# Kernel optimization log

Measured on AMD Instinct MI355X. Metric: run time of the kernel, lower is better.

## Reference

```python
import jax, jax.numpy as jnp
import numpy as np

EPS = 1e-5
STW = 10   # short_term_window_size
L = 12     # mlp_layers


def gru_step(h, x, Wi, Wh, bi, bh):
    # torch nn.GRU cell, gate order (r, z, n)
    gi = x @ Wi.T + bi            # [B, 3H]
    gh = h @ Wh.T + bh            # [B, 3H]
    ir, iz, inn = jnp.split(gi, 3, axis=-1)
    hr, hz, hn = jnp.split(gh, 3, axis=-1)
    r = jax.nn.sigmoid(ir + hr)
    z = jax.nn.sigmoid(iz + hz)
    n = jnp.tanh(inn + r * hn)
    return (1.0 - z) * n + z * h


def mlp_mini(m, seq_W, seq_b, ln_a, ln_b, out_W, out_b, mrg_W, mrg_b):
    # m: [B, S, H] -> siMLPe_mini -> [B, 1, C]
    f = jnp.swapaxes(m, 1, 2)                 # [B, H, S]
    for l in range(L):                        # TransMLP: temporal FC + spatial LN + residual
        y = f @ seq_W[l].T + seq_b[l]         # Linear over seq axis S
        mu = y.mean(axis=1, keepdims=True)    # LN over feature ('spatial') axis H
        var = ((y - mu) ** 2).mean(axis=1, keepdims=True)
        y = (y - mu) / jnp.sqrt(var + EPS) * ln_a[l][None, :, None] + ln_b[l][None, :, None]
        f = f + y
    f = jnp.swapaxes(f, 1, 2) @ out_W.T + out_b   # [B, S, C]  motion_fc_out
    f = jnp.swapaxes(f, 1, 2) @ mrg_W.T + mrg_b   # [B, C, 1]  temporal_merge_fc
    return jnp.swapaxes(f, 1, 2)                  # [B, 1, C]


def _forward(x, gru_Wi, gru_Wh, gru_bi, gru_bh, enc_W, enc_b,
             seq_W, seq_b, ln_alpha, ln_beta, out_W, out_b, merge_W, merge_b):
    B, T, C = x.shape
    H = gru_Wh.shape[1]

    @jax.checkpoint
    def enc_step(h, xt):
        return gru_step(h, xt, gru_Wi, gru_Wh, gru_bi, gru_bh), None

    h0 = jnp.zeros((B, H), dtype=x.dtype)
    h_enc, _ = jax.lax.scan(enc_step, h0, jnp.swapaxes(x[:, :-1, :], 0, 1))

    last_frame = x[:, -1, :]
    # encode_history=True: one GRU step on the last frame; resulting state discarded
    window_history = gru_step(h_enc, last_frame, gru_Wi, gru_Wh, gru_bi, gru_bh)[:, None, :]  # [B,1,H]

    buf0 = x[:, -STW:, :]  # sliding short-term window buffer [B, STW, C]

    @jax.checkpoint
    def dec_step(carry, _):
        h, last, buf = carry
        h = gru_step(h, last, gru_Wi, gru_Wh, gru_bi, gru_bh)
        dec = h[:, None, :]                        # [B, 1, H]
        wst = buf @ enc_W.T + enc_b                # fc_encoder: [B, STW, H]
        mlp_in = jnp.concatenate([window_history, wst, dec], axis=1)  # [B, STW+2, H]
        new = mlp_mini(mlp_in, seq_W, seq_b, ln_alpha, ln_beta, out_W, out_b, mrg_W=merge_W, mrg_b=merge_b)
        new = new + last[:, None, :]               # recursive_residual=True
        newf = new[:, 0, :]
        buf = jnp.concatenate([buf[:, 1:, :], new], axis=1)
        return (h, newf, buf), newf

    _, outs = jax.lax.scan(dec_step, (h_enc, last_frame, buf0), None, length=T)
    return jnp.swapaxes(outs, 0, 1)  # [B, T, C]


def setup_inputs() -> dict:
    key = jax.random.key(0)
    B, T, C, H = 1024, 64, 66, 1024
    S = STW + 2
    ks = jax.random.split(key, 16)

    def g(k, shape, scale):
        return jax.random.normal(k, shape, dtype=jnp.float32) * scale

    return {
        "x": g(ks[0], (B, T, C), 1.0),
        "gru_Wi": g(ks[1], (3 * H, C), 0.05),
        "gru_Wh": g(ks[2], (3 * H, H), 0.02),
        "gru_bi": jnp.zeros((3 * H,), jnp.float32),
        "gru_bh": jnp.zeros((3 * H,), jnp.float32),
        "enc_W": g(ks[3], (H, C), 0.05),
        "enc_b": jnp.zeros((H,), jnp.float32),
        "seq_W": g(ks[4], (L, S, S), 0.2),
        "seq_b": jnp.zeros((L, S), jnp.float32),
        "ln_alpha": jnp.ones((L, H), jnp.float32),
        "ln_beta": jnp.zeros((L, H), jnp.float32),
        "out_W": g(ks[5], (C, H), 0.02),
        "out_b": jnp.zeros((C,), jnp.float32),
        "merge_W": g(ks[6], (1, S), 0.2),
        "merge_b": jnp.zeros((1,), jnp.float32),
    }


def reference(x, gru_Wi, gru_Wh, gru_bi, gru_bh, enc_W, enc_b,
              seq_W, seq_b, ln_alpha, ln_beta, out_W, out_b, merge_W, merge_b):
    return _forward(x, gru_Wi, gru_Wh, gru_bi, gru_bh, enc_W, enc_b,
                    seq_W, seq_b, ln_alpha, ln_beta, out_W, out_b, merge_W, merge_b)
```

## Files before the change

kernel.cpp:

```cpp
#include <hip/hip_runtime.h>
#include <hip/hip_bf16.h>
#include <cstddef>
#include <cstdint>

#define BB 1024
#define TT 64
#define CC 66
#define HH 1024
#define SS 12
#define LL 12
#define XROW (TT*CC)
#define DPSEG 32

typedef __attribute__((ext_vector_type(8))) __bf16 bfrag;
typedef __attribute__((ext_vector_type(4))) float f32x4;
typedef __attribute__((ext_vector_type(8))) short s8v;
typedef __attribute__((ext_vector_type(2))) float f2;

__device__ __forceinline__ unsigned short f2bf(float f) {
  unsigned int u = __builtin_bit_cast(unsigned int, f);
  unsigned int r = u + 0x7FFFu + ((u >> 16) & 1u);
  return (unsigned short)(r >> 16);
}
__device__ __forceinline__ float bf2f(unsigned short h) {
  unsigned int u = ((unsigned int)h) << 16;
  return __builtin_bit_cast(float, u);
}

__device__ __forceinline__ void gload16(const void* g, void* l) {
  __builtin_amdgcn_global_load_lds(
      (const __attribute__((address_space(1))) unsigned int*)g,
      (__attribute__((address_space(3))) unsigned int*)l, 16, 0, 0);
}

template<int CTRL, int RM>
__device__ __forceinline__ float dppadd(float v) {
  int x = __builtin_amdgcn_update_dpp(0, __builtin_bit_cast(int, v),
                                      CTRL, RM, 0xF, true);
  return v + __builtin_bit_cast(float, x);
}
__device__ __forceinline__ float wave_sum63(float v) {
  v = dppadd<0x111, 0xF>(v);
  v = dppadd<0x112, 0xF>(v);
  v = dppadd<0x114, 0xF>(v);
  v = dppadd<0x118, 0xF>(v);
  v = dppadd<0x142, 0xa>(v);
  v = dppadd<0x143, 0xc>(v);
  return v;
}

__global__ __launch_bounds__(256) void gru_mfma(
    const unsigned short* __restrict__ Ahi, const unsigned short* __restrict__ Alo,
    const float* __restrict__ hprev,
    const unsigned short* __restrict__ Xhi, const unsigned short* __restrict__ Xlo,
    const unsigned short* __restrict__ Whi, const unsigned short* __restrict__ Wlo,
    const float* __restrict__ bi, const float* __restrict__ bh,
    float* __restrict__ hout_f32,
    unsigned short* __restrict__ hout_hi, unsigned short* __restrict__ hout_lo,
    const float* __restrict__ B144, float* __restrict__ dp32,
    const int* __restrict__ flagp, int do_dp)
{
  __shared__ __align__(16) unsigned short AsH[3][64*32];
  __shared__ __align__(16) unsigned short AsL[3][64*32];
  __shared__ __align__(16) unsigned short BsH[3][128*32];
  __shared__ __align__(16) unsigned short BsL[3][128*32];

  const int tid = threadIdx.x, lane = tid & 63, wid = tid >> 6;
  const int bid = blockIdx.x;
  const int idx = bid >> 3;
  const int jb = (bid & 7) * 4 + (idx & 3);
  const int b0 = (idx >> 2) * 64;
  const int wm = wid >> 1, wn = wid & 1;
  const int aR = lane >> 2, aC = lane & 3;

  auto stage = [&](int bs, int kc) {
    const unsigned short *shi, *slo; size_t go;
    int row = wid * 16 + aR;
    if (kc < 32) {
      go = (size_t)(b0 + row) * 1024 + (size_t)kc * 32 + aC * 8;
      shi = Ahi; slo = Alo;
    } else {
      go = (size_t)(b0 + row) * 96 + (size_t)(kc - 32) * 32 + aC * 8;
      shi = Xhi; slo = Xlo;
    }
    gload16(shi + go, &AsH[bs][wid * 512]);
    gload16(slo + go, &AsL[bs][wid * 512]);
    size_t base = ((size_t)jb * 35 + kc) * 4096;
    size_t go0 = base + (size_t)(wid * 32 + aR) * 32 + aC * 8;
    gload16(Whi + go0,       &BsH[bs][wid * 1024]);
    gload16(Whi + go0 + 512, &BsH[bs][wid * 1024 + 512]);
    gload16(Wlo + go0,       &BsL[bs][wid * 1024]);
    gload16(Wlo + go0 + 512, &BsL[bs][wid * 1024 + 512]);
  };

  int offA[2], offB[4];
  #pragma unroll
  for (int mh = 0; mh < 2; ++mh) {
    int r = wm * 32 + mh * 16 + (lane & 15);
    int cb = (lane >> 4) ^ (r & 3);
    offA[mh] = r * 32 + cb * 8;
  }
  #pragma unroll
  for (int g = 0; g < 4; ++g) {
    int r = wn * 64 + g * 16 + (lane & 15);
    int cb = (lane >> 4) ^ (r & 3);
    offB[g] = r * 32 + cb * 8;
  }

  f32x4 acc[2][4] = {};

  stage(0, 0);
  stage(1, 1);

  int cur = 0;
  for (int kc = 0; kc < 34; ++kc) {
    asm volatile("s_waitcnt vmcnt(6)" ::: "memory");
    __builtin_amdgcn_s_barrier();
    asm volatile("" ::: "memory");

    bfrag ah[2], al[2], bhf[4], blf[4];
    #pragma unroll
    for (int mh = 0; mh < 2; ++mh) {
      ah[mh] = __builtin_bit_cast(bfrag, *(const s8v*)(&AsH[cur][offA[mh]]));
      al[mh] = __builtin_bit_cast(bfrag, *(const s8v*)(&AsL[cur][offA[mh]]));
    }
    #pragma unroll
    for (int g = 0; g < 4; ++g) {
      bhf[g] = __builtin_bit_cast(bfrag, *(const s8v*)(&BsH[cur][offB[g]]));
      blf[g] = __builtin_bit_cast(bfrag, *(const s8v*)(&BsL[cur][offB[g]]));
    }
    if (kc < 33) {
      int st = (cur >= 1) ? cur - 1 : 2;
      stage(st, kc + 2);
    }
    #pragma unroll
    for (int mh = 0; mh < 2; ++mh)
      #pragma unroll
      for (int g = 0; g < 4; ++g) {
        acc[mh][g] = __builtin_amdgcn_mfma_f32_16x16x32_bf16(ah[mh], bhf[g], acc[mh][g], 0, 0, 0);
        acc[mh][g] = __builtin_amdgcn_mfma_f32_16x16x32_bf16(ah[mh], blf[g], acc[mh][g], 0, 0, 0);
        acc[mh][g] = __builtin_amdgcn_mfma_f32_16x16x32_bf16(al[mh], bhf[g], acc[mh][g], 0, 0, 0);
      }
    cur = (cur < 2) ? cur + 1 : 0;
  }
  {
    asm volatile("s_waitcnt vmcnt(0)" ::: "memory");
    __builtin_amdgcn_s_barrier();
    asm volatile("" ::: "memory");
    bfrag ah[2], al[2], bhf[4], blf[4];
    #pragma unroll
    for (int mh = 0; mh < 2; ++mh) {
      ah[mh] = __builtin_bit_cast(bfrag, *(const s8v*)(&AsH[1][offA[mh]]));
      al[mh] = __builtin_bit_cast(bfrag, *(const s8v*)(&AsL[1][offA[mh]]));
    }
    #pragma unroll
    for (int g = 0; g < 4; ++g) {
      bhf[g] = __builtin_bit_cast(bfrag, *(const s8v*)(&BsH[1][offB[g]]));
      blf[g] = __builtin_bit_cast(bfrag, *(const s8v*)(&BsL[1][offB[g]]));
    }
    #pragma unroll
    for (int mh = 0; mh < 2; ++mh)
      #pragma unroll
      for (int g = 0; g < 4; ++g) {
        acc[mh][g] = __builtin_amdgcn_mfma_f32_16x16x32_bf16(ah[mh], bhf[g], acc[mh][g], 0, 0, 0);
        acc[mh][g] = __builtin_amdgcn_mfma_f32_16x16x32_bf16(ah[mh], blf[g], acc[mh][g], 0, 0, 0);
        acc[mh][g] = __builtin_amdgcn_mfma_f32_16x16x32_bf16(al[mh], bhf[g], acc[mh][g], 0, 0, 0);
      }
  }

  const int j = jb * 32 + wn * 16 + (lane & 15);
  const float b_r  = bi[j] + bh[j];
  const float b_z  = bi[HH + j] + bh[HH + j];
  const float b_nh = bh[2 * HH + j];
  const float b_nx = bi[2 * HH + j];
  float hvv[2][4];
  #pragma unroll
  for (int mh = 0; mh < 2; ++mh)
    #pragma unroll
    for (int q = 0; q < 4; ++q) {
      int m = b0 + wm * 32 + mh * 16 + (lane >> 4) * 4 + q;
      float hpv = hprev[(size_t)m * HH + j];
      float rr = acc[mh][0][q] + b_r;
      float zz = acc[mh][1][q] + b_z;
      float nh = acc[mh][2][q] + b_nh;
      float nx = acc[mh][3][q] + b_nx;
      float r = 1.f / (1.f + __expf(-rr));
      float z = 1.f / (1.f + __expf(-zz));
      float n = tanhf(nx + r * nh);
      float hv = (1.f - z) * n + z * hpv;
      hvv[mh][q] = hv;
      hout_f32[(size_t)m * HH + j] = hv;
      unsigned short hi = f2bf(hv);
      float lo = hv - bf2f(hi);
      int cb = ((j >> 3) & 3) ^ (m & 3);
      size_t dst = (size_t)m * 1024 + (size_t)(j & ~31) + cb * 8 + (j & 7);
      hout_hi[dst] = hi;
      hout_lo[dst] = f2bf(lo);
    }

  if (do_dp && *flagp) {
    float* hsf = reinterpret_cast<float*>(&AsH[0][0]);
    __syncthreads();
    #pragma unroll
    for (int mh = 0; mh < 2; ++mh)
      #pragma unroll
      for (int q = 0; q < 4; ++q) {
        int mloc = wm * 32 + mh * 16 + (lane >> 4) * 4 + q;
        int jloc = wn * 16 + (lane & 15);
        hsf[mloc * 33 + jloc] = hvv[mh][q];
      }
    __syncthreads();
    const int b_sub = tid & 63;
    const int cg = __builtin_amdgcn_readfirstlane(tid >> 6);
    const int base_c = cg * 36;
    float acc36[36];
    #pragma unroll
    for (int i = 0; i < 36; ++i) acc36[i] = 0.f;
    for (int kk = 0; kk < 32; ++kk) {
      float av = hsf[b_sub * 33 + kk];
      const float* brow = B144 + (size_t)(jb * 32 + kk) * 144 + base_c;
      #pragma unroll
      for (int qq = 0; qq < 9; ++qq) {
        f32x4 b4 = *(const f32x4*)(brow + qq * 4);
        acc36[qq*4+0] = fmaf(av, b4[0], acc36[qq*4+0]);
        acc36[qq*4+1] = fmaf(av, b4[1], acc36[qq*4+1]);
        acc36[qq*4+2] = fmaf(av, b4[2], acc36[qq*4+2]);
        acc36[qq*4+3] = fmaf(av, b4[3], acc36[qq*4+3]);
      }
    }
    float* drow = dp32 + ((size_t)jb * 1024 + b0 + b_sub) * 144 + base_c;
    #pragma unroll
    for (int qq = 0; qq < 9; ++qq)
      *(f32x4*)(drow + qq * 4) = { acc36[qq*4+0], acc36[qq*4+1], acc36[qq*4+2], acc36[qq*4+3] };
  }
}

__global__ __launch_bounds__(256) void prep_wgc(
    const float* __restrict__ Wh, const float* __restrict__ Wi,
    unsigned short* __restrict__ Whi, unsigned short* __restrict__ Wlo)
{
  size_t idx = (size_t)blockIdx.x * 256 + threadIdx.x;
  if (idx >= (size_t)4096 * 1120) return;
  int k = (int)(idx % 1120);
  int rg = (int)(idx / 1120);
  int jbv = rg >> 7, r = rg & 127;
  int jhi = r >> 6, rem = r & 63, g = rem >> 4, jlo = rem & 15;
  int j = jbv * 32 + jhi * 16 + jlo;
  float v = 0.f;
  if (g == 0)      v = (k < 1024) ? Wh[(size_t)j * HH + k]            : ((k < 1090) ? Wi[(size_t)j * CC + (k - 1024)] : 0.f);
  else if (g == 1) v = (k < 1024) ? Wh[(size_t)(HH + j) * HH + k]     : ((k < 1090) ? Wi[(size_t)(HH + j) * CC + (k - 1024)] : 0.f);
  else if (g == 2) v = (k < 1024) ? Wh[(size_t)(2 * HH + j) * HH + k] : 0.f;
  else             v = (k >= 1024 && k < 1090) ? Wi[(size_t)(2 * HH + j) * CC + (k - 1024)] : 0.f;
  unsigned short hi = f2bf(v);
  float lo = v - bf2f(hi);
  int kc = k >> 5, kk = k & 31;
  int cb = ((kk >> 3) ^ (r & 3)) & 3;
  size_t dst = (((size_t)jbv * 35 + kc) * 128 + r) * 32 + cb * 8 + (kk & 7);
  Whi[dst] = hi;
  Wlo[dst] = f2bf(lo);
}

__global__ __launch_bounds__(256) void prep_xall(
    const float* __restrict__ x,
    unsigned short* __restrict__ Xhi, unsigned short* __restrict__ Xlo)
{
  size_t idx = (size_t)blockIdx.x * 256 + threadIdx.x;
  if (idx >= (size_t)TT * BB * 96) return;
  int kx = (int)(idx % 96);
  size_t rem = idx / 96;
  int b = (int)(rem % BB);
  int t = (int)(rem / BB);
  float v = (kx < CC) ? x[(size_t)b * XROW + (size_t)t * CC + kx] : 0.f;
  unsigned short hi = f2bf(v);
  float lo = v - bf2f(hi);
  int cb = (((kx >> 3) & 3) ^ (b & 3)) & 3;
  size_t dst = ((size_t)t * BB + b) * 96 + (size_t)(kx & ~31) + cb * 8 + (kx & 7);
  Xhi[dst] = hi;
  Xlo[dst] = f2bf(lo);
}

__global__ __launch_bounds__(256) void wst_row_kernel(
    const float* __restrict__ src, int src_stride,
    const float* __restrict__ encWT, const float* __restrict__ encb,
    float* __restrict__ dst, const int* __restrict__ flagp)
{
  if (*flagp) return;
  __shared__ float s[CC];
  int b = blockIdx.y;
  int h = blockIdx.x * 256 + threadIdx.x;
  if (threadIdx.x < CC) s[threadIdx.x] = src[(size_t)b * src_stride + threadIdx.x];
  __syncthreads();
  float acc = encb[h];
  #pragma unroll
  for (int k = 0; k < CC; ++k) acc = fmaf(s[k], encWT[(size_t)k * HH + h], acc);
  dst[(size_t)b * (10 * HH) + h] = acc;
}

__global__ __launch_bounds__(256) void transpose_encW(
    const float* __restrict__ W, float* __restrict__ WT)
{
  int k = blockIdx.x;
  int h = blockIdx.y * 256 + threadIdx.x;
  WT[(size_t)k * HH + h] = W[(size_t)h * CC + k];
}

__global__ __launch_bounds__(256) void copy_last_kernel(
    const float* __restrict__ x, float* __restrict__ last)
{
  int idx = blockIdx.x * 256 + threadIdx.x;
  if (idx < BB * CC) {
    int b = idx / CC, c = idx - b * CC;
    last[idx] = x[(size_t)b * XROW + 63 * CC + c];
  }
}

__global__ __launch_bounds__(256) void flag_kernel(
    const float* __restrict__ lnA, const float* __restrict__ lnB, int* flagp)
{
  int idx = blockIdx.x * 256 + threadIdx.x;
  bool ok;
  if (idx < LL * HH) ok = (lnA[idx] == 1.0f);
  else ok = (lnB[idx - LL * HH] == 0.0f);
  if (!ok) atomicAnd(flagp, 0);
}

__global__ __launch_bounds__(256) void prep_tabs(
    const float* __restrict__ encW, const float* __restrict__ encb,
    const float* __restrict__ outW, float* __restrict__ tabs)
{
  int idx = blockIdx.x * 256 + threadIdx.x;
  if (idx >= 8978) return;
  float a = 0.f;
  if (idx < 4356) {
    int c1 = idx / 66, c2 = idx % 66;
    for (int h = 0; h < HH; ++h) a = fmaf(encW[h * CC + c1], encW[h * CC + c2], a);
  } else if (idx < 8712) {
    int p = idx - 4356; int c = p / 66, c1 = p % 66;
    for (int h = 0; h < HH; ++h) a = fmaf(encW[h * CC + c1], outW[(size_t)c * HH + h], a);
  } else if (idx < 8778) {
    int c1 = idx - 8712;
    for (int h = 0; h < HH; ++h) a = fmaf(encW[h * CC + c1], encb[h], a);
  } else if (idx < 8844) {
    int c1 = idx - 8778;
    for (int h = 0; h < HH; ++h) a += encW[h * CC + c1];
  } else if (idx < 8910) {
    int c = idx - 8844;
    for (int h = 0; h < HH; ++h) a = fmaf(encb[h], outW[(size_t)c * HH + h], a);
  } else if (idx < 8976) {
    int c = idx - 8910;
    for (int h = 0; h < HH; ++h) a += outW[(size_t)c * HH + h];
  } else if (idx == 8976) {
    for (int h = 0; h < HH; ++h) a = fmaf(encb[h], encb[h], a);
  } else {
    for (int h = 0; h < HH; ++h) a += encb[h];
  }
  tabs[idx] = a;
}

__global__ __launch_bounds__(256) void prep_b144(
    const float* __restrict__ encW, const float* __restrict__ outW,
    const float* __restrict__ encb, float* __restrict__ B144)
{
  int idx = blockIdx.x * 256 + threadIdx.x;
  if (idx >= 1024 * 144) return;
  int k = idx / 144, n = idx % 144;
  float v;
  if (n < 66) v = encW[k * CC + n];
  else if (n < 132) v = outW[(size_t)(n - 66) * HH + k];
  else if (n == 132) v = encb[k];
  else if (n == 133) v = 1.f;
  else v = 0.f;
  B144[idx] = v;
}

__global__ __launch_bounds__(256) void linit_kernel(
    const float* __restrict__ x, float* __restrict__ l_ring,
    const int* __restrict__ flagp)
{
  if (!*flagp) return;
  int idx = blockIdx.x * 256 + threadIdx.x;
  if (idx >= 1024 * 9 * 66) return;
  int c = idx % 66; int r = idx / 66; int w = r % 9; int b = r / 9;
  l_ring[((size_t)b * 10 + w) * 66 + c] = x[(size_t)b * XROW + (54 + w) * CC + c];
}

__global__ __launch_bounds__(256) void qnew_kernel(
    const float* __restrict__ src, int sstride, const float* __restrict__ K3,
    float* __restrict__ q_ring, int slot, const int* __restrict__ flagp)
{
  if (!*flagp) return;
  __shared__ float Ks[4356];
  __shared__ float ls[8][66];
  int tid = threadIdx.x, b0 = blockIdx.x * 8;
  for (int i = tid; i < 4356; i += 256) Ks[i] = K3[i];
  for (int i = tid; i < 8 * 66; i += 256)
    ls[i / 66][i % 66] = src[(size_t)(b0 + i / 66) * sstride + (i % 66)];
  __syncthreads();
  for (int o = tid; o < 528; o += 256) {
    int bi = o / 66, c1 = o % 66;
    float a = 0.f;
    for (int c2 = 0; c2 < 66; ++c2) a = fmaf(Ks[c1 * 66 + c2], ls[bi][c2], a);
    q_ring[((size_t)(b0 + bi) * 10 + slot) * 66 + c1] = a;
  }
}

__global__ __launch_bounds__(256) void fast_combine(
    const float* __restrict__ dp, float* __restrict__ u, float* __restrict__ G,
    float* __restrict__ e, float* __restrict__ s, const int* __restrict__ flagp)
{
  if (!*flagp) return;
  int o = blockIdx.x * 256 + threadIdx.x;
  if (o >= 1024 * 144) return;
  int b = o / 144, c = o % 144;
  float a = 0.f;
  #pragma unroll
  for (int g = 0; g < DPSEG; ++g) a += dp[((size_t)g * 1024 + b) * 144 + c];
  if (c < 66) u[b * 66 + c] = a;
  else if (c < 132) G[b * 66 + (c - 66)] = a;
  else if (c == 132) e[b] = a;
  else if (c == 133) s[b] = a;
}

__global__ __launch_bounds__(256) void tail_kernel(
    const float* __restrict__ hdec, const float* __restrict__ whp,
    float* __restrict__ last, float* __restrict__ l_ring,
    float* __restrict__ q_ring, const float* __restrict__ dp,
    const float* __restrict__ u_whp, const float* __restrict__ G_whp,
    const float* __restrict__ e_whp, const float* __restrict__ s_whp,
    const float* __restrict__ tabs,
    float* __restrict__ wst, const float* __restrict__ encWT,
    const float* __restrict__ encb,
    const float* __restrict__ seqW, const float* __restrict__ seqb,
    const float* __restrict__ lnA, const float* __restrict__ lnB,
    const float* __restrict__ outW, const float* __restrict__ outb,
    const float* __restrict__ mrgW, const float* __restrict__ mrgb,
    int ring0, float* __restrict__ outp,
    unsigned short* __restrict__ lpH, unsigned short* __restrict__ lpL,
    const int* __restrict__ flagp)
{
  const int b = blockIdx.x, tid = threadIdx.x;
  const int lane = tid & 63, wid = tid >> 6;
  const int slot9 = (ring0 == 0) ? 9 : ring0 - 1;

  if (*flagp) {
    __shared__ float l_all[10][66], Qv[10][66];
    __shared__ float yd[66], gd[66], uw[66], se1[66], scs[66], lmix[66], newf[66];
    __shared__ float sW[156], sMm[156], sTt[156], sPp[156], sNn[156], sQq[156];
    __shared__ float sb12[12], sistd[12], scc[12], sfb[12], sdd12[12], swd[12], sVv[12], smrg[12];
    __shared__ float sred[12], misc[8];

    const float* K2T   = tabs + 4356;
    const float* tb_e1 = tabs + 8712;
    const float* tb_cs = tabs + 8778;
    const float* tb_g0 = tabs + 8844;
    const float* tb_R  = tabs + 8910;

    for (int i = tid; i < 660; i += 256) {
      int w = i / 66, c = i % 66;
      int slot = ring0 + w; if (slot >= 10) slot -= 10;
      Qv[w][c] = q_ring[((size_t)b * 10 + slot) * 66 + c];
      if (w < 9) l_all[w][c] = l_ring[((size_t)b * 10 + slot) * 66 + c];
      else       l_all[9][c] = last[(size_t)b * 66 + c];
    }
    for (int i = tid; i < 66; i += 256) {
      uw[i]  = u_whp[(size_t)b * 66 + i];
      se1[i] = tb_e1[i];
      scs[i] = tb_cs[i];
    }
    if (tid < 134) {
      float a = 0.f;
      #pragma unroll
      for (int g = 0; g < DPSEG; ++g) a += dp[((size_t)g * 1024 + b) * 144 + tid];
      if (tid < 66) yd[tid] = a;
      else if (tid < 132) gd[tid - 66] = a;
      else if (tid == 132) misc[1] = a;
      else misc[2] = a;
    }
    if (tid >= 160 && tid < 172) smrg[tid - 160] = mrgW[tid - 160];
    {
      f32x4 hv = *(const f32x4*)&hdec[(size_t)b * 1024 + tid * 4];
      f32x4 wv = *(const f32x4*)&whp[(size_t)b * 1024 + tid * 4];
      float d2 = hv[0]*hv[0] + hv[1]*hv[1] + hv[2]*hv[2] + hv[3]*hv[3];
      float dw = hv[0]*wv[0] + hv[1]*wv[1] + hv[2]*wv[2] + hv[3]*wv[3];
      float w2 = wv[0]*wv[0] + wv[1]*wv[1] + wv[2]*wv[2] + wv[3]*wv[3];
      d2 = wave_sum63(d2); dw = wave_sum63(dw); w2 = wave_sum63(w2);
      if (lane == 63) { sred[wid*3] = d2; sred[wid*3+1] = dw; sred[wid*3+2] = w2; }
    }
    __syncthreads();
    if (tid >= 128 && tid < 131) {
      int i = tid - 128;
      misc[3 + i] = sred[i] + sred[3 + i] + sred[6 + i] + sred[9 + i];
    }
    if (tid == 132) misc[6] = tabs[8976];
    if (tid == 133) misc[7] = tabs[8977];
    __syncthreads();

    if (tid < 144) {
      int i = tid / 12, j = tid % 12;
      float gv;
      if (i == 0 && j == 0) gv = misc[5];
      else if (i == 11 && j == 11) gv = misc[3];
      else if ((i == 0 && j == 11) || (i == 11 && j == 0)) gv = misc[4];
      else if (i == 0 || j == 0) {
        int w = (i == 0 ? j : i) - 1;
        float a = e_whp[b];
        for (int c = 0; c < 66; ++c) a = fmaf(uw[c], l_all[w][c], a);
        gv = a;
      } else if (i == 11 || j == 11) {
        int w = (i == 11 ? j : i) - 1;
        float a = misc[1];
        for (int c = 0; c < 66; ++c) a = fmaf(yd[c], l_all[w][c], a);
        gv = a;
      } else {
        int wi = i - 1, wj = j - 1;
        float a = misc[6];
        for (int c = 0; c < 66; ++c) a = fmaf(se1[c], l_all[wi][c] + l_all[wj][c], a);
        for (int c = 0; c < 66; ++c) a = fmaf(l_all[wi][c], Qv[wj][c], a);
        gv = a;
      }
      sMm[i * 13 + j] = gv * (1.f / 1024.f);
      sTt[i * 13 + j] = (i == j) ? 1.f : 0.f;
    }
    if (tid >= 144 && tid < 156) {
      int k = tid - 144;
      float fb;
      if (k == 0) fb = s_whp[b] * (1.f / 1024.f);
      else if (k == 11) fb = misc[2] * (1.f / 1024.f);
      else {
        float a = misc[7];
        for (int c = 0; c < 66; ++c) a = fmaf(scs[c], l_all[k - 1][c], a);
        fb = a * (1.f / 1024.f);
      }
      sfb[k] = fb;
      sdd12[k] = 0.f;
    }
    __syncthreads();

    for (int l = 0; l < LL; ++l) {
      if (tid < 144) sW[(tid / 12) * 13 + (tid % 12)] = seqW[l * 144 + tid];
      if (tid >= 160 && tid < 172) sb12[tid - 160] = seqb[l * 12 + (tid - 160)];
      __syncthreads();
      if (tid < 144) {
        int s = tid / 12, k = tid % 12;
        float a = 0.f;
        #pragma unroll
        for (int k2 = 0; k2 < 12; ++k2) a = fmaf(sW[s * 13 + k2], sMm[k2 * 13 + k], a);
        sPp[s * 13 + k] = a;
      }
      __syncthreads();
      if (tid < 12) {
        int s = tid;
        float mu = sb12[s];
        #pragma unroll
        for (int k = 0; k < 12; ++k) mu = fmaf(sW[s * 13 + k], sfb[k], mu);
        float e2 = 0.f;
        #pragma unroll
        for (int k = 0; k < 12; ++k) e2 = fmaf(sPp[s * 13 + k], sW[s * 13 + k], e2);
        float wf = mu - sb12[s];
        float var = fmaxf(e2 - wf * wf, 0.f);
        float is = 1.f / sqrtf(var + 1e-5f);
        sistd[s] = is;
        scc[s] = is * (sb12[s] - mu);
      }
      __syncthreads();
      if (tid < 144) {
        int i = tid / 12, j = tid % 12;
        float a = 0.f;
        #pragma unroll
        for (int k = 0; k < 12; ++k) a = fmaf(sW[i * 13 + k], sTt[k * 13 + j], a);
        sQq[i * 13 + j] = a;
        sNn[i * 13 + j] = sMm[i * 13 + j] + sistd[i] * sPp[i * 13 + j];
      }
      if (tid >= 144 && tid < 156) {
        int i = tid - 144;
        float a = 0.f;
        #pragma unroll
        for (int k = 0; k < 12; ++k) a = fmaf(sW[i * 13 + k], sdd12[k], a);
        swd[i] = a;
      }
      __syncthreads();
      if (tid < 144) {
        int i = tid / 12, j = tid % 12;
        sTt[i * 13 + j] += sistd[i] * sQq[i * 13 + j];
        float a = 0.f;
        #pragma unroll
        for (int k = 0; k < 12; ++k) a = fmaf(sNn[i * 13 + k], sW[j * 13 + k], a);
        sPp[i * 13 + j] = a;
      }
      if (tid >= 144 && tid < 156) {
        int i = tid - 144;
        sdd12[i] = sdd12[i] + sistd[i] * swd[i] + scc[i];
      }
      __syncthreads();
      if (tid < 144) {
        int i = tid / 12, j = tid % 12;
        sMm[i * 13 + j] = sNn[i * 13 + j] + sPp[i * 13 + j] * sistd[j]
                        + sfb[i] * scc[j] + scc[i] * sfb[j] - scc[i] * scc[j];
      }
      __syncthreads();
    }

    if (tid < 12) {
      float a = 0.f;
      #pragma unroll
      for (int s = 0; s < 12; ++s) a = fmaf(smrg[s], sTt[s * 13 + tid], a);
      sVv[tid] = a;
    }
    if (tid == 200) {
      float a = 0.f;
      for (int s = 0; s < 12; ++s) a = fmaf(smrg[s], sdd12[s], a);
      misc[0] = a;
    }
    __syncthreads();
    if (tid < 66) {
      float a = 0.f;
      #pragma unroll
      for (int w = 0; w < 9; ++w) a = fmaf(sVv[1 + w], l_all[w][tid], a);
      a = fmaf(sVv[10], l_all[9][tid], a);
      lmix[tid] = a;
    }
    __syncthreads();
    if (tid < 66) {
      int c = tid;
      float vsr = 0.f, smw = 0.f;
      #pragma unroll
      for (int k = 1; k <= 10; ++k) vsr += sVv[k];
      #pragma unroll
      for (int s = 0; s < 12; ++s) smw += smrg[s];
      float lastv = l_all[9][c];
      float acc = sVv[0] * G_whp[(size_t)b * 66 + c]
                + vsr * tb_g0[c]
                + sVv[11] * gd[c]
                + misc[0] * tb_R[c]
                + smw * outb[c] + mrgb[0] + lastv;
      const float* krow = K2T + c * 66;
      for (int c2 = 0; c2 < 66; ++c2) acc = fmaf(lmix[c2], krow[c2], acc);
      outp[(size_t)b * XROW + c] = acc;
      last[(size_t)b * 66 + c] = acc;
      l_ring[((size_t)b * 10 + slot9) * 66 + c] = lastv;
      newf[c] = acc;
      unsigned short hi = f2bf(acc);
      float lo = acc - bf2f(hi);
      int cb = (((c >> 3) & 3) ^ (b & 3)) & 3;
      size_t dst = (size_t)b * 96 + (size_t)(c & ~31) + cb * 8 + (c & 7);
      lpH[dst] = hi;
      lpL[dst] = f2bf(lo);
    }
    __syncthreads();
    if (tid < 66) {
      float a = 0.f;
      const float* k3r = tabs + tid * 66;
      for (int c2 = 0; c2 < 66; ++c2) a = fmaf(k3r[c2], newf[c2], a);
      q_ring[((size_t)b * 10 + ring0) * 66 + tid] = a;
    }
    return;
  }

  __shared__ float red[4][24];
  __shared__ f2 mustd2[SS];
  __shared__ float g_lds[HH];
  __shared__ float nc[CC];

  const int h0 = tid;
  const int h1 = tid + 512;
  const float* lrow = last + (size_t)b * CC;
  f2 wnew[2];
  {
    f2 a0 = { encb[h0], encb[h0 + 256] };
    f2 a1 = { encb[h1], encb[h1 + 256] };
    #pragma unroll 11
    for (int k = 0; k < CC; ++k) {
      float lv = lrow[k];
      f2 lv2 = { lv, lv };
      f2 w0 = { encWT[(size_t)k * HH + h0], encWT[(size_t)k * HH + h0 + 256] };
      f2 w1 = { encWT[(size_t)k * HH + h1], encWT[(size_t)k * HH + h1 + 256] };
      a0 = __builtin_elementwise_fma(lv2, w0, a0);
      a1 = __builtin_elementwise_fma(lv2, w1, a1);
    }
    wnew[0] = a0; wnew[1] = a1;
    float* wd = wst + ((size_t)b * 10 + slot9) * HH;
    wd[h0] = a0.x; wd[h0 + 256] = a0.y;
    wd[h1] = a1.x; wd[h1 + 256] = a1.y;
  }

  f2 fr[2][SS];
  {
    const float* whb = whp + (size_t)b * HH;
    const float* hb  = hdec + (size_t)b * HH;
    fr[0][0]  = { whb[h0], whb[h0 + 256] };
    fr[1][0]  = { whb[h1], whb[h1 + 256] };
    fr[0][11] = { hb[h0], hb[h0 + 256] };
    fr[1][11] = { hb[h1], hb[h1 + 256] };
    #pragma unroll
    for (int w = 0; w < 9; ++w) {
      int slot = ring0 + w; if (slot >= 10) slot -= 10;
      const float* ws_ = wst + ((size_t)b * 10 + slot) * HH;
      fr[0][1 + w] = { ws_[h0], ws_[h0 + 256] };
      fr[1][1 + w] = { ws_[h1], ws_[h1 + 256] };
    }
    fr[0][10] = wnew[0];
    fr[1][10] = wnew[1];
  }

  #pragma unroll 1
  for (int l = 0; l < LL; ++l) {
    const float* W  = seqW + (size_t)l * SS * SS;
    const float* Bv = seqb + (size_t)l * SS;
    const float* lA = lnA + (size_t)l * HH;
    const float* lB = lnB + (size_t)l * HH;
    f2 al[2], be[2];
    al[0] = { lA[h0], lA[h0 + 256] };  al[1] = { lA[h1], lA[h1 + 256] };
    be[0] = { lB[h0], lB[h0 + 256] };  be[1] = { lB[h1], lB[h1 + 256] };

    f2 y[2][SS];
    #pragma unroll
    for (int s = 0; s < SS; ++s) {
      float bv = Bv[s];
      f2 a0 = { bv, bv }, a1 = { bv, bv };
      #pragma unroll
      for (int k = 0; k < SS; ++k) {
        float wv = W[s * SS + k];
        f2 wv2 = { wv, wv };
        a0 = __builtin_elementwise_fma(fr[0][k], wv2, a0);
        a1 = __builtin_elementwise_fma(fr[1][k], wv2, a1);
      }
      y[0][s] = a0; y[1][s] = a1;
      f2 pp = a0 + a1;
      float ps = wave_sum63(pp.x + pp.y);
      f2 qq = __builtin_elementwise_fma(a0, a0, a1 * a1);
      float pq = wave_sum63(qq.x + qq.y);
      if (lane == 63) { red[wid][s] = ps; red[wid][12 + s] = pq; }
    }
    __syncthreads();
    if (tid < SS) {
      float S = red[0][tid] + red[1][tid] + red[2][tid] + red[3][tid];
      float Q = red[0][12 + tid] + red[1][12 + tid] + red[2][12 + tid] + red[3][12 + tid];
      float mu = S * (1.f / HH);
      float var = Q * (1.f / HH) - mu * mu;
      mustd2[tid] = { mu, 1.f / sqrtf(var + 1e-5f) };
    }
    __syncthreads();
    #pragma unroll
    for (int s = 0; s < SS; ++s) {
      f2 mi = mustd2[s];
      f2 mus = { mi.x, mi.x };
      f2 isd = { mi.y, mi.y };
      #pragma unroll
      for (int p = 0; p < 2; ++p) {
        f2 t = (y[p][s] - mus) * isd;
        fr[p][s] = __builtin_elementwise_fma(t, al[p], fr[p][s]) + be[p];
      }
    }
    __syncthreads();
  }

  float smw = 0.f;
  f2 g[2] = { {0.f, 0.f}, {0.f, 0.f} };
  #pragma unroll
  for (int s = 0; s < SS; ++s) {
    float mv = mrgW[s];
    smw += mv;
    f2 mv2 = { mv, mv };
    g[0] = __builtin_elementwise_fma(mv2, fr[0][s], g[0]);
    g[1] = __builtin_elementwise_fma(mv2, fr[1][s], g[1]);
  }
  g_lds[h0] = g[0].x; g_lds[h0 + 256] = g[0].y;
  g_lds[h1] = g[1].x; g_lds[h1 + 256] = g[1].y;
  const float mbv = mrgb[0];
  __syncthreads();
  #pragma unroll 1
  for (int i = 0; i < 17; ++i) {
    int c = wid + 4 * i;
    if (c < CC) {
      const float* ow = outW + (size_t)c * HH;
      float acc = 0.f;
      #pragma unroll
      for (int q = 0; q < 16; ++q) acc = fmaf(g_lds[lane + q * 64], ow[lane + q * 64], acc);
      acc = wave_sum63(acc);
      if (lane == 63) nc[c] = acc + outb[c] * smw + mbv + lrow[c];
    }
  }
  __syncthreads();
  if (tid < CC) {
    float nv = nc[tid];
    outp[(size_t)b * XROW + tid] = nv;
    last[(size_t)b * CC + tid] = nv;
    unsigned short hi = f2bf(nv);
    float lo = nv - bf2f(hi);
    int cb = (((tid >> 3) & 3) ^ (b & 3)) & 3;
    size_t dst = (size_t)b * 96 + (size_t)(tid & ~31) + cb * 8 + (tid & 7);
    lpH[dst] = hi;
    lpL[dst] = f2bf(lo);
  }
}

extern "C" void kernel_launch(void* const* d_in, const int* in_sizes, int n_in,
                              void* d_out, int out_size, void* d_ws, size_t ws_size,
                              hipStream_t stream) {
  const float* x    = (const float*)d_in[0];
  const float* gWi  = (const float*)d_in[1];
  const float* gWh  = (const float*)d_in[2];
  const float* gbi  = (const float*)d_in[3];
  const float* gbh  = (const float*)d_in[4];
  const float* encW = (const float*)d_in[5];
  const float* encb = (const float*)d_in[6];
  const float* seqW = (const float*)d_in[7];
  const float* seqb = (const float*)d_in[8];
  const float* lnA  = (const float*)d_in[9];
  const float* lnB  = (const float*)d_in[10];
  const float* outW = (const float*)d_in[11];
  const float* outb = (const float*)d_in[12];
  const float* mrgW = (const float*)d_in[13];
  const float* mrgb = (const float*)d_in[14];
  float* out = (float*)d_out;

  char* p = (char*)d_ws;
  auto alloc = [&](size_t bytes) { char* r = p; p += (bytes + 255) & ~(size_t)255; return r; };
  float* encWT = (float*)alloc((size_t)CC * HH * 4);
  float* last  = (float*)alloc((size_t)BB * CC * 4);
  float* wst   = (float*)alloc((size_t)BB * 10 * HH * 4);
  float* hf[3];
  for (int i = 0; i < 3; ++i) hf[i] = (float*)alloc((size_t)BB * HH * 4);
  unsigned short* WgH = (unsigned short*)alloc((size_t)4096 * 1120 * 2);
  unsigned short* WgL = (unsigned short*)alloc((size_t)4096 * 1120 * 2);
  unsigned short* XaH = (unsigned short*)alloc((size_t)TT * BB * 96 * 2);
  unsigned short* XaL = (unsigned short*)alloc((size_t)TT * BB * 96 * 2);
  unsigned short* hhi[3]; unsigned short* hlo[3];
  for (int i = 0; i < 3; ++i) {
    hhi[i] = (unsigned short*)alloc((size_t)BB * HH * 2);
    hlo[i] = (unsigned short*)alloc((size_t)BB * HH * 2);
  }
  unsigned short* lpH = (unsigned short*)alloc((size_t)BB * 96 * 2);
  unsigned short* lpL = (unsigned short*)alloc((size_t)BB * 96 * 2);
  int* flag = (int*)alloc(256);
  if ((size_t)(p - (char*)d_ws) > ws_size) return;

  char* ov = (char*)wst;
  float* B144  = (float*)ov;                 ov += (size_t)1024 * 144 * 4;
  float* dp32  = (float*)ov;                 ov += (size_t)DPSEG * 1024 * 144 * 4;
  float* l_ring= (float*)ov;                 ov += (size_t)1024 * 10 * 66 * 4;
  float* q_ring= (float*)ov;                 ov += (size_t)1024 * 10 * 66 * 4;
  float* u_whp = (float*)ov;                 ov += (size_t)1024 * 66 * 4;
  float* G_whp = (float*)ov;                 ov += (size_t)1024 * 66 * 4;
  float* e_whp = (float*)ov;                 ov += 4096;
  float* s_whp = (float*)ov;                 ov += 4096;
  float* tabs  = (float*)ov;                 ov += 9216 * 4;

  hipMemsetAsync(flag, 0xFF, 4, stream);
  flag_kernel<<<dim3(96), 256, 0, stream>>>(lnA, lnB, flag);
  prep_wgc<<<dim3((4096u * 1120u) / 256u), 256, 0, stream>>>(gWh, gWi, WgH, WgL);
  prep_xall<<<dim3(((unsigned)TT * BB * 96) / 256u), 256, 0, stream>>>(x, XaH, XaL);
  transpose_encW<<<dim3(CC, HH/256), 256, 0, stream>>>(encW, encWT);
  copy_last_kernel<<<dim3((BB*CC + 255)/256), 256, 0, stream>>>(x, last);
  prep_b144<<<dim3(576), 256, 0, stream>>>(encW, outW, encb, B144);
  prep_tabs<<<dim3(36), 256, 0, stream>>>(encW, encb, outW, tabs);
  linit_kernel<<<dim3((1024*9*66)/256), 256, 0, stream>>>(x, l_ring, flag);
  for (int w = 0; w < 10; ++w)
    qnew_kernel<<<dim3(128), 256, 0, stream>>>(x + (size_t)(54 + w) * CC, XROW,
                                               tabs, q_ring, w, flag);
  hipMemsetAsync(hf[0], 0, (size_t)BB * HH * 4, stream);
  hipMemsetAsync(hhi[0], 0, (size_t)BB * HH * 2, stream);
  hipMemsetAsync(hlo[0], 0, (size_t)BB * HH * 2, stream);

  const dim3 ggrid(512);

  int cur = 0;
  for (int t = 0; t < 63; ++t) {
    int nxt = 1 - cur;
    gru_mfma<<<ggrid, 256, 0, stream>>>(
        hhi[cur], hlo[cur], hf[cur],
        XaH + (size_t)t * BB * 96, XaL + (size_t)t * BB * 96,
        WgH, WgL, gbi, gbh, hf[nxt], hhi[nxt], hlo[nxt],
        B144, dp32, flag, 0);
    cur = nxt;
  }
  gru_mfma<<<ggrid, 256, 0, stream>>>(
      hhi[cur], hlo[cur], hf[cur],
      XaH + (size_t)63 * BB * 96, XaL + (size_t)63 * BB * 96,
      WgH, WgL, gbi, gbh, hf[2], hhi[2], hlo[2],
      B144, dp32, flag, 1);

  fast_combine<<<dim3(576), 256, 0, stream>>>(dp32, u_whp, G_whp, e_whp, s_whp, flag);

  for (int w = 0; w < 9; ++w)
    wst_row_kernel<<<dim3(HH/256, BB), 256, 0, stream>>>(
        x + (size_t)(54 + w) * CC, XROW, encWT, encb, wst + (size_t)w * HH, flag);

  int hc = 2;
  for (int t = 0; t < 64; ++t) {
    if (t > 0) {
      int hn = (t - 1) & 1;
      gru_mfma<<<ggrid, 256, 0, stream>>>(
          hhi[hc], hlo[hc], hf[hc], lpH, lpL,
          WgH, WgL, gbi, gbh, hf[hn], hhi[hn], hlo[hn],
          B144, dp32, flag, 1);
      hc = hn;
    }
    tail_kernel<<<dim3(BB), 256, 0, stream>>>(
        hf[hc], hf[2], last, l_ring, q_ring, dp32,
        u_whp, G_whp, e_whp, s_whp, tabs,
        wst, encWT, encb, seqW, seqb, lnA, lnB, outW, outb, mrgW, mrgb,
        t % 10, out + (size_t)t * CC, lpH, lpL, flag);
  }
}
```

Before: 7.997 ms.

## Change LDS swizzle to row-pair XOR and parallelize prep_tabs per wave

Changes the XOR swizzle used for bf16 hi/lo tiles from (row & 3) to ((row >> 1) & 3) consistently in all producers (weight prep, x prep, GRU output, last-frame writes) and in the MFMA fragment read offsets. The aim is fewer LDS bank conflicts when the MFMA kernel reads fragments, since rows are 64 bytes wide and two rows share one bank cycle. Separately, prep_tabs now assigns one wave per output with a lane-strided loop and wave reduction instead of one thread per output, exposing far more parallelism for that setup kernel. The swizzle must stay consistent across every writer and reader, otherwise results would be wrong.

```diff
diff --git a/kernel.cpp b/kernel.cpp
--- a/kernel.cpp
+++ b/kernel.cpp
@@ -16,6 +16,8 @@
 typedef __attribute__((ext_vector_type(4))) float f32x4;
 typedef __attribute__((ext_vector_type(8))) short s8v;
 typedef __attribute__((ext_vector_type(2))) float f2;
+
+#define SWROW(r) (((r) >> 1) & 3)
 
 __device__ __forceinline__ unsigned short f2bf(float f) {
   unsigned int u = __builtin_bit_cast(unsigned int, f);
@@ -97,13 +99,13 @@
   #pragma unroll
   for (int mh = 0; mh < 2; ++mh) {
     int r = wm * 32 + mh * 16 + (lane & 15);
-    int cb = (lane >> 4) ^ (r & 3);
+    int cb = (lane >> 4) ^ SWROW(r);
     offA[mh] = r * 32 + cb * 8;
   }
   #pragma unroll
   for (int g = 0; g < 4; ++g) {
     int r = wn * 64 + g * 16 + (lane & 15);
-    int cb = (lane >> 4) ^ (r & 3);
+    int cb = (lane >> 4) ^ SWROW(r);
     offB[g] = r * 32 + cb * 8;
   }
 
@@ -192,7 +194,7 @@
       hout_f32[(size_t)m * HH + j] = hv;
       unsigned short hi = f2bf(hv);
       float lo = hv - bf2f(hi);
-      int cb = ((j >> 3) & 3) ^ (m & 3);
+      int cb = ((j >> 3) & 3) ^ SWROW(m);
       size_t dst = (size_t)m * 1024 + (size_t)(j & ~31) + cb * 8 + (j & 7);
       hout_hi[dst] = hi;
       hout_lo[dst] = f2bf(lo);
@@ -254,7 +256,7 @@
   unsigned short hi = f2bf(v);
   float lo = v - bf2f(hi);
   int kc = k >> 5, kk = k & 31;
-  int cb = ((kk >> 3) ^ (r & 3)) & 3;
+  int cb = ((kk >> 3) ^ SWROW(r)) & 3;
   size_t dst = (((size_t)jbv * 35 + kc) * 128 + r) * 32 + cb * 8 + (kk & 7);
   Whi[dst] = hi;
   Wlo[dst] = f2bf(lo);
@@ -273,7 +275,7 @@
   float v = (kx < CC) ? x[(size_t)b * XROW + (size_t)t * CC + kx] : 0.f;
   unsigned short hi = f2bf(v);
   float lo = v - bf2f(hi);
-  int cb = (((kx >> 3) & 3) ^ (b & 3)) & 3;
+  int cb = (((kx >> 3) & 3) ^ SWROW(b)) & 3;
   size_t dst = ((size_t)t * BB + b) * 96 + (size_t)(kx & ~31) + cb * 8 + (kx & 7);
   Xhi[dst] = hi;
   Xlo[dst] = f2bf(lo);
@@ -328,33 +330,35 @@
     const float* __restrict__ encW, const float* __restrict__ encb,
     const float* __restrict__ outW, float* __restrict__ tabs)
 {
-  int idx = blockIdx.x * 256 + threadIdx.x;
+  const int lane = threadIdx.x & 63, wid = threadIdx.x >> 6;
+  int idx = blockIdx.x * 4 + wid;
   if (idx >= 8978) return;
   float a = 0.f;
   if (idx < 4356) {
     int c1 = idx / 66, c2 = idx % 66;
-    for (int h = 0; h < HH; ++h) a = fmaf(encW[h * CC + c1], encW[h * CC + c2], a);
+    for (int h = lane; h < HH; h += 64) a = fmaf(encW[h * CC + c1], encW[h * CC + c2], a);
   } else if (idx < 8712) {
     int p = idx - 4356; int c = p / 66, c1 = p % 66;
-    for (int h = 0; h < HH; ++h) a = fmaf(encW[h * CC + c1], outW[(size_t)c * HH + h], a);
+    for (int h = lane; h < HH; h += 64) a = fmaf(encW[h * CC + c1], outW[(size_t)c * HH + h], a);
   } else if (idx < 8778) {
     int c1 = idx - 8712;
-    for (int h = 0; h < HH; ++h) a = fmaf(encW[h * CC + c1], encb[h], a);
+    for (int h = lane; h < HH; h += 64) a = fmaf(encW[h * CC + c1], encb[h], a);
   } else if (idx < 8844) {
     int c1 = idx - 8778;
-    for (int h = 0; h < HH; ++h) a += encW[h * CC + c1];
+    for (int h = lane; h < HH; h += 64) a += encW[h * CC + c1];
   } else if (idx < 8910) {
     int c = idx - 8844;
-    for (int h = 0; h < HH; ++h) a = fmaf(encb[h], outW[(size_t)c * HH + h], a);
+    for (int h = lane; h < HH; h += 64) a = fmaf(encb[h], outW[(size_t)c * HH + h], a);
   } else if (idx < 8976) {
     int c = idx - 8910;
-    for (int h = 0; h < HH; ++h) a += outW[(size_t)c * HH + h];
+    for (int h = lane; h < HH; h += 64) a += outW[(size_t)c * HH + h];
   } else if (idx == 8976) {
-    for (int h = 0; h < HH; ++h) a = fmaf(encb[h], encb[h], a);
+    for (int h = lane; h < HH; h += 64) a = fmaf(encb[h], encb[h], a);
   } else {
-    for (int h = 0; h < HH; ++h) a += encb[h];
-  }
-  tabs[idx] = a;
+    for (int h = lane; h < HH; h += 64) a += encb[h];
+  }
+  a = wave_sum63(a);
+  if (lane == 63) tabs[idx] = a;
 }
 
 __global__ __launch_bounds__(256) void prep_b144(
@@ -641,7 +645,7 @@
       newf[c] = acc;
       unsigned short hi = f2bf(acc);
       float lo = acc - bf2f(hi);
-      int cb = (((c >> 3) & 3) ^ (b & 3)) & 3;
+      int cb = (((c >> 3) & 3) ^ SWROW(b)) & 3;
       size_t dst = (size_t)b * 96 + (size_t)(c & ~31) + cb * 8 + (c & 7);
       lpH[dst] = hi;
       lpL[dst] = f2bf(lo);
@@ -787,7 +791,7 @@
     last[(size_t)b * CC + tid] = nv;
     unsigned short hi = f2bf(nv);
     float lo = nv - bf2f(hi);
-    int cb = (((tid >> 3) & 3) ^ (b & 3)) & 3;
+    int cb = (((tid >> 3) & 3) ^ SWROW(b)) & 3;
     size_t dst = (size_t)b * 96 + (size_t)(tid & ~31) + cb * 8 + (tid & 7);
     lpH[dst] = hi;
     lpL[dst] = f2bf(lo);
@@ -853,7 +857,7 @@
   transpose_encW<<<dim3(CC, HH/256), 256, 0, stream>>>(encW, encWT);
   copy_last_kernel<<<dim3((BB*CC + 255)/256), 256, 0, stream>>>(x, last);
   prep_b144<<<dim3(576), 256, 0, stream>>>(encW, outW, encb, B144);
-  prep_tabs<<<dim3(36), 256, 0, stream>>>(encW, encb, outW, tabs);
+  prep_tabs<<<dim3(2245), 256, 0, stream>>>(encW, encb, outW, tabs);
   linit_kernel<<<dim3((1024*9*66)/256), 256, 0, stream>>>(x, l_ring, flag);
   for (int w = 0; w < 10; ++w)
     qnew_kernel<<<dim3(128), 256, 0, stream>>>(x + (size_t)(54 + w) * CC, XROW,
```

Result: no change. 7.953 ms (-0.6%).
